# Kernel tuning notes

Measured on AMD Instinct MI355X. Metric: run time of the kernel, lower is better.

The kernel has to match this reference:

```python
import jax, jax.numpy as jnp
import numpy as np

N, L, S, H, D = 2, 4096, 4096, 8, 32


def setup_inputs() -> dict:
    key = jax.random.key(0)
    kq, kk, kv, km = jax.random.split(key, 4)
    queries = jax.random.normal(kq, (N, L, H, D), dtype=jnp.float32)
    keys = jax.random.normal(kk, (N, S, H, D), dtype=jnp.float32)
    values = jax.random.normal(kv, (N, S, H, D), dtype=jnp.float32)
    q_mask = jnp.ones((N, L), dtype=bool)
    kv_mask = jax.random.randint(km, (N, S), 0, 2).astype(bool)
    return {"queries": queries, "keys": keys, "values": values,
            "q_mask": q_mask, "kv_mask": kv_mask}


def reference(queries, keys, values, q_mask, kv_mask):
    # QK: [N, L, S, H] -- contraction over head dim D (GEMM form of the
    # original broadcast-multiply-sum).
    QK = jnp.einsum('nlhd,nshd->nlsh', queries, keys)
    mask = q_mask[:, :, None] & kv_mask[:, None, :]            # [N, L, S]
    QK = jnp.where(mask[..., None], QK, -jnp.inf)
    softmax_temp = 1.0 / np.sqrt(D).astype(np.float32)
    A = jax.nn.softmax(softmax_temp * QK, axis=2)              # softmax over S
    # weighted value sum: [N, L, H, D]
    return jnp.einsum('nlsh,nshd->nlhd', A, values)
```

## Files before the change

kernel.cpp:

```cpp
#include <hip/hip_runtime.h>
#include <stdint.h>
#include <math.h>


typedef __bf16 bf16x8 __attribute__((ext_vector_type(8)));
typedef float  f32x16 __attribute__((ext_vector_type(16)));
typedef float  f32x4  __attribute__((ext_vector_type(4)));

#define C2 0.25502407414058425f

#define IDX_OFF_I 16
#define BUF_OFF_B 32832

__global__ void prep_compact(const int* __restrict__ KM, int* __restrict__ W) {
    const int n = blockIdx.x;
    const int tid = threadIdx.x, lane = tid & 63, wv = tid >> 6;
    const int* m = KM + n * 4096;
    __shared__ int csum[64];
    for (int c = wv; c < 64; c += 4) {
        unsigned long long bal = __ballot(m[c * 64 + lane] != 0);
        if (lane == 0) csum[c] = __popcll(bal);
    }
    __syncthreads();
    if (wv == 0) {
        int v = csum[lane];
        #pragma unroll
        for (int off = 1; off < 64; off <<= 1) {
            int u = __shfl_up(v, off);
            if (lane >= off) v += u;
        }
        csum[lane] = v;
        if (lane == 63) W[n] = v;
    }
    __syncthreads();
    const int total = csum[63];
    int* idxp = W + IDX_OFF_I + n * 4096;
    for (int c = wv; c < 64; c += 4) {
        bool mm = m[c * 64 + lane] != 0;
        unsigned long long bal = __ballot(mm);
        int base = c ? csum[c - 1] : 0;
        int pre = __popcll(bal & ((1ull << lane) - 1ull));
        if (mm) idxp[base + pre] = c * 64 + lane;
    }
    const int cnt32 = (total + 31) & ~31;
    for (int j = total + tid; j < cnt32; j += 256) idxp[j] = 0;
}

__global__ __launch_bounds__(256) void prep_gather(
    const float* __restrict__ K, const float* __restrict__ V,
    const int* __restrict__ W, __bf16* __restrict__ BUF)
{
    const int wib = threadIdx.x >> 6, lane = threadIdx.x & 63;
    const int gt = blockIdx.x * 4 + wib;
    const int n = gt >> 10, h = (gt >> 7) & 7, t = gt & 127;
    const int cnt = W[n];
    if (t >= ((cnt + 31) >> 5)) return;
    const int hi = lane >> 5, lq = lane & 31;
    const int* idx = W + IDX_OFF_I + n * 4096;
    const float* Kb = K + (size_t)n * 4096 * 256 + h * 32;
    const float* Vb = V + (size_t)n * 4096 * 256 + h * 32;
    __bf16* dst = BUF + (size_t)gt * 2048 + lane * 8;

    const float* krow = Kb + (size_t)idx[t * 32 + lq] * 256 + 8 * hi;
    #pragma unroll
    for (int f = 0; f < 2; ++f) {
        f32x4 a = *(const f32x4*)(krow + 16 * f);
        f32x4 b = *(const f32x4*)(krow + 16 * f + 4);
        bf16x8 o8;
        o8[0] = (__bf16)a[0]; o8[1] = (__bf16)a[1]; o8[2] = (__bf16)a[2]; o8[3] = (__bf16)a[3];
        o8[4] = (__bf16)b[0]; o8[5] = (__bf16)b[1]; o8[6] = (__bf16)b[2]; o8[7] = (__bf16)b[3];
        *(bf16x8*)(dst + f * 512) = o8;
    }
    #pragma unroll
    for (int f = 0; f < 2; ++f) {
        bf16x8 o8;
        #pragma unroll
        for (int j = 0; j < 8; ++j) {
            int s = t * 32 + 16 * f + (j & 3) + 4 * hi + 8 * ((j >> 2) & 1);
            o8[j] = (__bf16)Vb[(size_t)idx[s] * 256 + lq];
        }
        *(bf16x8*)(dst + 1024 + f * 512) = o8;
    }
}

__global__ __launch_bounds__(256, 4) void fattn32(
    const float* __restrict__ Q, const __bf16* __restrict__ BUF,
    const int* __restrict__ W, float* __restrict__ Out)
{
    constexpr int L = 4096, H = 8, D = 32, RS = H * D;
    const int lane = threadIdx.x & 63;
    const int wib  = threadIdx.x >> 6;
    const int w    = (blockIdx.x & 7) * 256 + (blockIdx.x >> 3);
    const int qt   = w & 127;
    const int h    = (w >> 7) & 7;
    const int n    = w >> 10;
    const int hi   = lane >> 5;
    const int lq   = lane & 31;

    const int cnt    = W[n];
    const int ntiles = (cnt + 31) >> 5;

    const float* qrow = Q + ((size_t)n * L + qt * 32 + lq) * RS + h * D + 8 * hi;
    bf16x8 qf[2];
    #pragma unroll
    for (int f = 0; f < 2; ++f) {
        f32x4 a = *(const f32x4*)(qrow + 16 * f);
        f32x4 b = *(const f32x4*)(qrow + 16 * f + 4);
        bf16x8 ff;
        ff[0] = (__bf16)(C2 * a[0]); ff[1] = (__bf16)(C2 * a[1]);
        ff[2] = (__bf16)(C2 * a[2]); ff[3] = (__bf16)(C2 * a[3]);
        ff[4] = (__bf16)(C2 * b[0]); ff[5] = (__bf16)(C2 * b[1]);
        ff[6] = (__bf16)(C2 * b[2]); ff[7] = (__bf16)(C2 * b[3]);
        qf[f] = ff;
    }

    const __bf16* bufp = BUF + (size_t)((n * 8 + h) * 128) * 2048 + lane * 8;

    f32x16 o = {};
    float l = 0.0f;
    const f32x16 z = {};

    for (int t = wib; t < ntiles; t += 4) {
        const __bf16* tb = bufp + (size_t)t * 2048;
        bf16x8 kf0 = *(const bf16x8*)(tb);
        bf16x8 kf1 = *(const bf16x8*)(tb + 512);
        bf16x8 vf0 = *(const bf16x8*)(tb + 1024);
        bf16x8 vf1 = *(const bf16x8*)(tb + 1536);

        f32x16 st = __builtin_amdgcn_mfma_f32_32x32x16_bf16(kf0, qf[0], z, 0, 0, 0);
        st = __builtin_amdgcn_mfma_f32_32x32x16_bf16(kf1, qf[1], st, 0, 0, 0);

        float p[16];
        #pragma unroll
        for (int r = 0; r < 16; ++r)
            p[r] = __builtin_amdgcn_exp2f(st[r]);

        const int kb = t * 32;
        if (kb + 32 > cnt) {
            #pragma unroll
            for (int r = 0; r < 16; ++r) {
                int ks = kb + (r & 3) + 8 * ((r >> 2) & 1) + 16 * (r >> 3) + 4 * hi;
                if (ks >= cnt) p[r] = 0.0f;
            }
        }

        l += (((p[0] + p[1]) + (p[2] + p[3])) + ((p[4] + p[5]) + (p[6] + p[7])))
           + (((p[8] + p[9]) + (p[10] + p[11])) + ((p[12] + p[13]) + (p[14] + p[15])));

        bf16x8 pf0, pf1;
        #pragma unroll
        for (int j = 0; j < 8; ++j) { pf0[j] = (__bf16)p[j]; pf1[j] = (__bf16)p[8 + j]; }

        o = __builtin_amdgcn_mfma_f32_32x32x16_bf16(vf0, pf0, o, 0, 0, 0);
        o = __builtin_amdgcn_mfma_f32_32x32x16_bf16(vf1, pf1, o, 0, 0, 0);
    }

    __shared__ float xt[4][32 * 33];
    __shared__ float Ls[4][32];

    float lt = l + __shfl_xor(l, 32);
    float* tp = xt[wib];
    #pragma unroll
    for (int r = 0; r < 16; ++r) {
        int d = (r & 3) + 8 * (r >> 2) + 4 * hi;
        tp[lq * 33 + d] = o[r];
    }
    if (hi == 0) Ls[wib][lq] = lt;
    __syncthreads();

    const int q  = threadIdx.x >> 3;
    const int dg = (threadIdx.x & 7) * 4;
    float ltot = Ls[0][q] + Ls[1][q] + Ls[2][q] + Ls[3][q];
    float inv = 1.0f / ltot;
    f32x4 acc = {};
    #pragma unroll
    for (int wv = 0; wv < 4; ++wv) {
        #pragma unroll
        for (int jj = 0; jj < 4; ++jj)
            acc[jj] += xt[wv][q * 33 + dg + jj];
    }
    acc[0] *= inv; acc[1] *= inv; acc[2] *= inv; acc[3] *= inv;
    float* orow = Out + (((size_t)(n * L + qt * 32 + q)) * H + h) * D + dg;
    *(f32x4*)orow = acc;
}

extern "C" void kernel_launch(void* const* d_in, const int* in_sizes, int n_in,
                              void* d_out, int out_size, void* d_ws, size_t ws_size,
                              hipStream_t stream) {
    const float* Q = (const float*)d_in[0];
    const float* K = (const float*)d_in[1];
    const float* V = (const float*)d_in[2];
    const int* KM = (const int*)d_in[4];
    float* Out = (float*)d_out;

    int* Wk = (int*)d_ws;
    __bf16* BUF = (__bf16*)((char*)d_ws + BUF_OFF_B);

    hipLaunchKernelGGL(prep_compact, dim3(2),   dim3(256), 0, stream, KM, Wk);
    hipLaunchKernelGGL(prep_gather,  dim3(512), dim3(256), 0, stream, K, V, Wk, BUF);
    hipLaunchKernelGGL(fattn32,      dim3(2048), dim3(256), 0, stream, Q, BUF, Wk, Out);
}
```

Baseline: 47.23 us.

## Fuse mask compaction into gather kernel, prefetch next KV tile, raise occupancy

Merges the two prep kernels into one. Each gather block now recomputes the kv-mask prefix-sum compaction into shared memory, which removes a kernel launch and the global index round trip. The attention loop now software-prefetches the next K/V tile into registers while computing the current one. Launch bounds are raised to 8 waves-per-EU occupancy. The costs are redundant mask scanning in every one of 512 blocks, plus extra register pressure under a tighter register budget.

```diff
diff --git a/kernel.cpp b/kernel.cpp
--- a/kernel.cpp
+++ b/kernel.cpp
@@ -9,20 +9,24 @@
 
 #define C2 0.25502407414058425f
 
-#define IDX_OFF_I 16
-#define BUF_OFF_B 32832
-
-__global__ void prep_compact(const int* __restrict__ KM, int* __restrict__ W) {
-    const int n = blockIdx.x;
-    const int tid = threadIdx.x, lane = tid & 63, wv = tid >> 6;
+#define BUF_OFF_B 64
+
+__global__ __launch_bounds__(256) void prep(
+    const float* __restrict__ K, const float* __restrict__ V,
+    const int* __restrict__ KM, int* __restrict__ W, __bf16* __restrict__ BUF)
+{
+    const int wib = threadIdx.x >> 6, lane = threadIdx.x & 63;
+    const int n = blockIdx.x >> 8;
+    __shared__ int csum[64];
+    __shared__ int idx[4096];
+
     const int* m = KM + n * 4096;
-    __shared__ int csum[64];
-    for (int c = wv; c < 64; c += 4) {
+    for (int c = wib; c < 64; c += 4) {
         unsigned long long bal = __ballot(m[c * 64 + lane] != 0);
         if (lane == 0) csum[c] = __popcll(bal);
     }
     __syncthreads();
-    if (wv == 0) {
+    if (wib == 0) {
         int v = csum[lane];
         #pragma unroll
         for (int off = 1; off < 64; off <<= 1) {
@@ -30,33 +34,26 @@
             if (lane >= off) v += u;
         }
         csum[lane] = v;
-        if (lane == 63) W[n] = v;
     }
     __syncthreads();
     const int total = csum[63];
-    int* idxp = W + IDX_OFF_I + n * 4096;
-    for (int c = wv; c < 64; c += 4) {
+    for (int c = wib; c < 64; c += 4) {
         bool mm = m[c * 64 + lane] != 0;
         unsigned long long bal = __ballot(mm);
         int base = c ? csum[c - 1] : 0;
         int pre = __popcll(bal & ((1ull << lane) - 1ull));
-        if (mm) idxp[base + pre] = c * 64 + lane;
+        if (mm) idx[base + pre] = c * 64 + lane;
     }
     const int cnt32 = (total + 31) & ~31;
-    for (int j = total + tid; j < cnt32; j += 256) idxp[j] = 0;
-}
-
-__global__ __launch_bounds__(256) void prep_gather(
-    const float* __restrict__ K, const float* __restrict__ V,
-    const int* __restrict__ W, __bf16* __restrict__ BUF)
-{
-    const int wib = threadIdx.x >> 6, lane = threadIdx.x & 63;
+    for (int j = total + (int)threadIdx.x; j < cnt32; j += 256) idx[j] = 0;
+    __syncthreads();
+
+    if (threadIdx.x == 0 && (blockIdx.x & 255) == 0) W[n] = total;
+
     const int gt = blockIdx.x * 4 + wib;
-    const int n = gt >> 10, h = (gt >> 7) & 7, t = gt & 127;
-    const int cnt = W[n];
-    if (t >= ((cnt + 31) >> 5)) return;
+    const int h = (gt >> 7) & 7, t = gt & 127;
+    if (t >= ((total + 31) >> 5)) return;
     const int hi = lane >> 5, lq = lane & 31;
-    const int* idx = W + IDX_OFF_I + n * 4096;
     const float* Kb = K + (size_t)n * 4096 * 256 + h * 32;
     const float* Vb = V + (size_t)n * 4096 * 256 + h * 32;
     __bf16* dst = BUF + (size_t)gt * 2048 + lane * 8;
@@ -83,7 +80,7 @@
     }
 }
 
-__global__ __launch_bounds__(256, 4) void fattn32(
+__global__ __launch_bounds__(256, 8) void fattn32(
     const float* __restrict__ Q, const __bf16* __restrict__ BUF,
     const int* __restrict__ W, float* __restrict__ Out)
 {
@@ -101,17 +98,19 @@
     const int ntiles = (cnt + 31) >> 5;
 
     const float* qrow = Q + ((size_t)n * L + qt * 32 + lq) * RS + h * D + 8 * hi;
-    bf16x8 qf[2];
-    #pragma unroll
-    for (int f = 0; f < 2; ++f) {
-        f32x4 a = *(const f32x4*)(qrow + 16 * f);
-        f32x4 b = *(const f32x4*)(qrow + 16 * f + 4);
-        bf16x8 ff;
-        ff[0] = (__bf16)(C2 * a[0]); ff[1] = (__bf16)(C2 * a[1]);
-        ff[2] = (__bf16)(C2 * a[2]); ff[3] = (__bf16)(C2 * a[3]);
-        ff[4] = (__bf16)(C2 * b[0]); ff[5] = (__bf16)(C2 * b[1]);
-        ff[6] = (__bf16)(C2 * b[2]); ff[7] = (__bf16)(C2 * b[3]);
-        qf[f] = ff;
+    bf16x8 qf0, qf1;
+    {
+        f32x4 a0 = *(const f32x4*)(qrow);
+        f32x4 b0 = *(const f32x4*)(qrow + 4);
+        f32x4 a1 = *(const f32x4*)(qrow + 16);
+        f32x4 b1 = *(const f32x4*)(qrow + 20);
+        #pragma unroll
+        for (int j = 0; j < 4; ++j) {
+            qf0[j]     = (__bf16)(C2 * a0[j]);
+            qf0[4 + j] = (__bf16)(C2 * b0[j]);
+            qf1[j]     = (__bf16)(C2 * a1[j]);
+            qf1[4 + j] = (__bf16)(C2 * b1[j]);
+        }
     }
 
     const __bf16* bufp = BUF + (size_t)((n * 8 + h) * 128) * 2048 + lane * 8;
@@ -120,15 +119,23 @@
     float l = 0.0f;
     const f32x16 z = {};
 
-    for (int t = wib; t < ntiles; t += 4) {
-        const __bf16* tb = bufp + (size_t)t * 2048;
-        bf16x8 kf0 = *(const bf16x8*)(tb);
-        bf16x8 kf1 = *(const bf16x8*)(tb + 512);
-        bf16x8 vf0 = *(const bf16x8*)(tb + 1024);
-        bf16x8 vf1 = *(const bf16x8*)(tb + 1536);
-
-        f32x16 st = __builtin_amdgcn_mfma_f32_32x32x16_bf16(kf0, qf[0], z, 0, 0, 0);
-        st = __builtin_amdgcn_mfma_f32_32x32x16_bf16(kf1, qf[1], st, 0, 0, 0);
+    int t = wib;
+    const __bf16* tb = bufp + (size_t)t * 2048;
+    bf16x8 ck0 = *(const bf16x8*)(tb);
+    bf16x8 ck1 = *(const bf16x8*)(tb + 512);
+    bf16x8 cv0 = *(const bf16x8*)(tb + 1024);
+    bf16x8 cv1 = *(const bf16x8*)(tb + 1536);
+
+    for (; t < ntiles; t += 4) {
+        const int tn = (t + 4 < ntiles) ? t + 4 : t;
+        const __bf16* nb = bufp + (size_t)tn * 2048;
+        bf16x8 nk0 = *(const bf16x8*)(nb);
+        bf16x8 nk1 = *(const bf16x8*)(nb + 512);
+        bf16x8 nv0 = *(const bf16x8*)(nb + 1024);
+        bf16x8 nv1 = *(const bf16x8*)(nb + 1536);
+
+        f32x16 st = __builtin_amdgcn_mfma_f32_32x32x16_bf16(ck0, qf0, z, 0, 0, 0);
+        st = __builtin_amdgcn_mfma_f32_32x32x16_bf16(ck1, qf1, st, 0, 0, 0);
 
         float p[16];
         #pragma unroll
@@ -151,8 +158,10 @@
         #pragma unroll
         for (int j = 0; j < 8; ++j) { pf0[j] = (__bf16)p[j]; pf1[j] = (__bf16)p[8 + j]; }
 
-        o = __builtin_amdgcn_mfma_f32_32x32x16_bf16(vf0, pf0, o, 0, 0, 0);
-        o = __builtin_amdgcn_mfma_f32_32x32x16_bf16(vf1, pf1, o, 0, 0, 0);
+        o = __builtin_amdgcn_mfma_f32_32x32x16_bf16(cv0, pf0, o, 0, 0, 0);
+        o = __builtin_amdgcn_mfma_f32_32x32x16_bf16(cv1, pf1, o, 0, 0, 0);
+
+        ck0 = nk0; ck1 = nk1; cv0 = nv0; cv1 = nv1;
     }
 
     __shared__ float xt[4][32 * 33];
@@ -196,7 +205,6 @@
     int* Wk = (int*)d_ws;
     __bf16* BUF = (__bf16*)((char*)d_ws + BUF_OFF_B);
 
-    hipLaunchKernelGGL(prep_compact, dim3(2),   dim3(256), 0, stream, KM, Wk);
-    hipLaunchKernelGGL(prep_gather,  dim3(512), dim3(256), 0, stream, K, V, Wk, BUF);
-    hipLaunchKernelGGL(fattn32,      dim3(2048), dim3(256), 0, stream, Q, BUF, Wk, Out);
+    hipLaunchKernelGGL(prep,    dim3(512),  dim3(256), 0, stream, K, V, KM, Wk, BUF);
+    hipLaunchKernelGGL(fattn32, dim3(2048), dim3(256), 0, stream, Q, BUF, Wk, Out);
 }
```

New measurement: 110.2 us. 2.33x slower.
